# Kernel tuning notes

Hardware: AMD Instinct MI355X
Metric: run time of the kernel (lower is better)

Reference implementation:

```python
import jax, jax.numpy as jnp
import numpy as np

N = 1048576        # rows
F = 16             # categorical features
C = 1024           # num_classes per feature (uniform)


def setup_inputs() -> dict:
    key = jax.random.key(0)
    k_idx, k_cb, k_gb = jax.random.split(key, 3)
    inputs = jax.random.randint(k_idx, (N, F), 0, C, dtype=jnp.int64)
    # class_bias[i] in torch is [C, 1]; stacked here as [F, C]
    class_bias = jax.random.normal(k_cb, (F, C), dtype=jnp.float32)
    # global_bias[i] in torch is [1, 1]; stacked here as [F]
    global_bias = jax.random.normal(k_gb, (F,), dtype=jnp.float32)
    return {"inputs": inputs, "class_bias": class_bias, "global_bias": global_bias}


def reference(inputs, class_bias, global_bias):
    # Torch computes one_hot(inputs[:, i], C) @ class_bias[i] + global_bias[i]
    # per feature, then hstack + squeeze -> [N, F]. The one_hot+matmul is
    # mathematically an exact row gather: class_bias[i][inputs[:, i]].
    feat_ids = jnp.arange(F)[None, :]          # [1, F]
    gathered = class_bias[feat_ids, inputs]    # [N, F] advanced-index gather
    return gathered + global_bias[None, :]     # [N, F]
```

## Files before the change

### kernel.cpp

```cpp
#include <hip/hip_runtime.h>


constexpr int kC = 1024;
constexpr int kF = 16;
constexpr int kTab = kF * kC;

typedef int   v4i __attribute__((ext_vector_type(4)));
typedef float v4f __attribute__((ext_vector_type(4)));

__global__ __launch_bounds__(1024, 8) void onehot_lds_kernel(
    const v4i* __restrict__ idx4,
    const v4f* __restrict__ cb4,
    const float* __restrict__ gb,
    v4f* __restrict__ out4,
    int total4)
{
    __shared__ float lut[kTab];

    {
        v4f* lut4 = (v4f*)lut;
        #pragma unroll
        for (int j = 0; j < 4; ++j) {
            int p = threadIdx.x + j * 1024;
            v4f v = cb4[p];
            float b = gb[p >> 8];
            v.x += b; v.y += b; v.z += b; v.w += b;
            lut4[p] = v;
        }
    }
    __syncthreads();

    const int S = gridDim.x * blockDim.x;
    int t = blockIdx.x * blockDim.x + threadIdx.x;
    const int f0 = (t & 3) << 2;
    const float* __restrict__ base = lut + f0 * kC;

    for (; t + 3 * S < total4; t += 4 * S) {
        v4i a0 = __builtin_nontemporal_load(&idx4[t]);
        v4i a1 = __builtin_nontemporal_load(&idx4[t + S]);
        v4i a2 = __builtin_nontemporal_load(&idx4[t + 2 * S]);
        v4i a3 = __builtin_nontemporal_load(&idx4[t + 3 * S]);
        v4f o0, o1, o2, o3;
        o0.x = base[a0.x]; o0.y = base[kC + a0.y]; o0.z = base[2 * kC + a0.z]; o0.w = base[3 * kC + a0.w];
        o1.x = base[a1.x]; o1.y = base[kC + a1.y]; o1.z = base[2 * kC + a1.z]; o1.w = base[3 * kC + a1.w];
        o2.x = base[a2.x]; o2.y = base[kC + a2.y]; o2.z = base[2 * kC + a2.z]; o2.w = base[3 * kC + a2.w];
        o3.x = base[a3.x]; o3.y = base[kC + a3.y]; o3.z = base[2 * kC + a3.z]; o3.w = base[3 * kC + a3.w];
        __builtin_nontemporal_store(o0, &out4[t]);
        __builtin_nontemporal_store(o1, &out4[t + S]);
        __builtin_nontemporal_store(o2, &out4[t + 2 * S]);
        __builtin_nontemporal_store(o3, &out4[t + 3 * S]);
    }
    for (; t < total4; t += S) {
        v4i a = __builtin_nontemporal_load(&idx4[t]);
        v4f o;
        o.x = base[a.x]; o.y = base[kC + a.y]; o.z = base[2 * kC + a.z]; o.w = base[3 * kC + a.w];
        __builtin_nontemporal_store(o, &out4[t]);
    }
}

extern "C" void kernel_launch(void* const* d_in, const int* in_sizes, int n_in,
                              void* d_out, int out_size, void* d_ws, size_t ws_size,
                              hipStream_t stream) {
    const v4i* idx4 = (const v4i*)d_in[0];
    const v4f* cb4  = (const v4f*)d_in[1];
    const float* gb = (const float*)d_in[2];
    v4f* out4 = (v4f*)d_out;

    const int total4 = out_size / 4;
    const int block  = 1024;
    const int grid   = 512;
    onehot_lds_kernel<<<grid, block, 0, stream>>>(idx4, cb4, gb, out4, total4);
}
```

Before: 29.12 us.

## Prefetch first index batch before LUT build and software-pipeline index loads

The first two index vectors are now loaded before the shared-memory table is filled, so global-load latency overlaps the LUT setup. The main loop is software-pipelined: it loads the next pair of index vectors while gathering and storing the current pair, replacing the four-wide unrolled loop. The occupancy hint on launch_bounds is dropped. This costs extra live registers and leaves fewer loads in flight per iteration.

New measurement: 27.83 us. 1.05x faster.

```diff
diff --git a/kernel.cpp b/kernel.cpp
--- a/kernel.cpp
+++ b/kernel.cpp
@@ -8,7 +8,7 @@
 typedef int   v4i __attribute__((ext_vector_type(4)));
 typedef float v4f __attribute__((ext_vector_type(4)));
 
-__global__ __launch_bounds__(1024, 8) void onehot_lds_kernel(
+__global__ __launch_bounds__(1024) void onehot_lds_kernel(
     const v4i* __restrict__ idx4,
     const v4f* __restrict__ cb4,
     const float* __restrict__ gb,
@@ -16,6 +16,18 @@
     int total4)
 {
     __shared__ float lut[kTab];
+
+    const int S = gridDim.x * blockDim.x;
+    int t = blockIdx.x * blockDim.x + threadIdx.x;
+    const int f0 = (t & 3) << 2;
+    const float* __restrict__ base = lut + f0 * kC;
+
+    v4i a0, a1;
+    bool have = (t + S) < total4;
+    if (have) {
+        a0 = __builtin_nontemporal_load(&idx4[t]);
+        a1 = __builtin_nontemporal_load(&idx4[t + S]);
+    }
 
     {
         v4f* lut4 = (v4f*)lut;
@@ -30,30 +42,28 @@
     }
     __syncthreads();
 
-    const int S = gridDim.x * blockDim.x;
-    int t = blockIdx.x * blockDim.x + threadIdx.x;
-    const int f0 = (t & 3) << 2;
-    const float* __restrict__ base = lut + f0 * kC;
-
-    for (; t + 3 * S < total4; t += 4 * S) {
-        v4i a0 = __builtin_nontemporal_load(&idx4[t]);
-        v4i a1 = __builtin_nontemporal_load(&idx4[t + S]);
-        v4i a2 = __builtin_nontemporal_load(&idx4[t + 2 * S]);
-        v4i a3 = __builtin_nontemporal_load(&idx4[t + 3 * S]);
-        v4f o0, o1, o2, o3;
-        o0.x = base[a0.x]; o0.y = base[kC + a0.y]; o0.z = base[2 * kC + a0.z]; o0.w = base[3 * kC + a0.w];
-        o1.x = base[a1.x]; o1.y = base[kC + a1.y]; o1.z = base[2 * kC + a1.z]; o1.w = base[3 * kC + a1.w];
-        o2.x = base[a2.x]; o2.y = base[kC + a2.y]; o2.z = base[2 * kC + a2.z]; o2.w = base[3 * kC + a2.w];
-        o3.x = base[a3.x]; o3.y = base[kC + a3.y]; o3.z = base[2 * kC + a3.z]; o3.w = base[3 * kC + a3.w];
+    while (have) {
+        const int tn = t + 2 * S;
+        const bool haven = (tn + S) < total4;
+        v4i b0, b1;
+        if (haven) {
+            b0 = __builtin_nontemporal_load(&idx4[tn]);
+            b1 = __builtin_nontemporal_load(&idx4[tn + S]);
+        }
+        v4f o0, o1;
+        o0.x = base[a0.x]; o0.y = base[kC + a0.y];
+        o0.z = base[2 * kC + a0.z]; o0.w = base[3 * kC + a0.w];
         __builtin_nontemporal_store(o0, &out4[t]);
+        o1.x = base[a1.x]; o1.y = base[kC + a1.y];
+        o1.z = base[2 * kC + a1.z]; o1.w = base[3 * kC + a1.w];
         __builtin_nontemporal_store(o1, &out4[t + S]);
-        __builtin_nontemporal_store(o2, &out4[t + 2 * S]);
-        __builtin_nontemporal_store(o3, &out4[t + 3 * S]);
+        t = tn; a0 = b0; a1 = b1; have = haven;
     }
     for (; t < total4; t += S) {
         v4i a = __builtin_nontemporal_load(&idx4[t]);
         v4f o;
-        o.x = base[a.x]; o.y = base[kC + a.y]; o.z = base[2 * kC + a.z]; o.w = base[3 * kC + a.w];
+        o.x = base[a.x]; o.y = base[kC + a.y];
+        o.z = base[2 * kC + a.z]; o.w = base[3 * kC + a.w];
         __builtin_nontemporal_store(o, &out4[t]);
     }
 }
```
